# Kernel optimization log

Hardware: AMD Instinct MI355X
Metric: run time of the kernel (lower is better)

Reference implementation:

```python
import jax, jax.numpy as jnp
import numpy as np

G, N, EPG = 32, 128, 2048   # graphs, nodes/graph (uniform), edges/graph
H, L = 128, 2               # hidden_dim, num_layers
OUT = 12


def setup_inputs() -> dict:
    key = jax.random.key(0)
    ks = jax.random.split(key, 32)
    x = jax.random.randint(ks[0], (G * N, 9), 0, 2, dtype=jnp.int32)
    edge_attr = jax.random.randint(ks[1], (G * EPG, 3), 0, 2, dtype=jnp.int32)
    # edges stay within their own graph (global ids = local + graph offset)
    src = jax.random.randint(ks[2], (G, EPG), 0, N, dtype=jnp.int32)
    dst = jax.random.randint(ks[3], (G, EPG), 0, N, dtype=jnp.int32)
    off = (jnp.arange(G, dtype=jnp.int32) * N)[:, None]
    edge_index = jnp.stack([(src + off).reshape(-1), (dst + off).reshape(-1)]).astype(jnp.int64)
    batch_idx = (jnp.arange(G * N) // N).astype(jnp.int32)

    def p(k, shape, scale=0.05):
        return jax.random.normal(k, shape, dtype=jnp.float32) * scale

    return dict(
        x=x, edge_index=edge_index, edge_attr=edge_attr, batch_idx=batch_idx,
        atom_tab=p(ks[4], (9, 119, H)), bond_tab=p(ks[5], (3, 8, H)),
        W_m1=p(ks[6], (L, 2 * H, H)), b_m1=jnp.zeros((L, H), jnp.float32),
        W_m2=p(ks[7], (L, 2 * H, H)), b_m2=jnp.zeros((L, H), jnp.float32),
        W_me=p(ks[8], (L, H, H)), b_me=jnp.zeros((L, H), jnp.float32),
        W_mg=p(ks[9], (L, H, H)), b_mg=jnp.zeros((L, H), jnp.float32),
        W_h1=p(ks[10], (L, H, H)), b_h1=jnp.zeros((L, H), jnp.float32),
        W_h2=p(ks[11], (L, H, H)), b_h2=jnp.zeros((L, H), jnp.float32),
        W_o1=p(ks[12], (L, 2 * H, H)), b_o1=jnp.zeros((L, H), jnp.float32),
        W_o2=p(ks[13], (L, H, H)), b_o2=jnp.zeros((L, H), jnp.float32),
        Wg1=p(ks[14], (H, H)), bg1=jnp.zeros((H,), jnp.float32),
        Wg2=p(ks[15], (H, OUT)), bg2=jnp.zeros((OUT,), jnp.float32),
    )


def reference(x, edge_index, edge_attr, batch_idx, atom_tab, bond_tab,
              W_m1, b_m1, W_m2, b_m2, W_me, b_me, W_mg, b_mg,
              W_h1, b_h1, W_h2, b_h2, W_o1, b_o1, W_o2, b_o2,
              Wg1, bg1, Wg2, bg2):
    # Atom/Bond encoders: sum of per-feature embeddings
    node_fts = jnp.sum(jax.vmap(lambda t, i: t[i], in_axes=(0, 1))(atom_tab, x), axis=0)        # (G*N, H)
    edge_fts = jnp.sum(jax.vmap(lambda t, i: t[i], in_axes=(0, 1))(bond_tab, edge_attr), axis=0)  # (E, H)

    # dense adjacency + dense edge features (one fused scatter, replaces per-graph loop)
    g = (edge_index[0] // N).astype(jnp.int32)
    s = (edge_index[0] % N).astype(jnp.int32)
    d = (edge_index[1] % N).astype(jnp.int32)
    adj = jnp.zeros((G, N, N), jnp.float32).at[g, s, d].set(1.0)
    edense = jnp.zeros((G, N, N, H), jnp.float32).at[g, s, d].set(edge_fts)

    nd = node_fts.reshape(G, N, H)          # to_dense_batch (uniform graphs -> no padding)
    gf = jnp.zeros((G, H), jnp.float32)
    hid = jnp.zeros_like(nd)
    NEG = jnp.float32(-1e9)

    for l in range(L):  # CLRS MPNN layers
        z = jnp.concatenate([nd, hid], axis=-1)                 # (G, N, 2H)
        m1 = z @ W_m1[l] + b_m1[l]
        m2 = z @ W_m2[l] + b_m2[l]
        me = edense @ W_me[l] + b_me[l]                         # (G, N, N, H)
        mg = gf @ W_mg[l] + b_mg[l]
        msgs = m1[:, None, :, :] + m2[:, :, None, :] + me + mg[:, None, None, :]
        h = jax.nn.relu(msgs)
        h = jax.nn.relu(h @ W_h1[l] + b_h1[l]) @ W_h2[l] + b_h2[l]
        h = jnp.where(adj[..., None] > 0, h, NEG)               # masked max over senders
        agg = jnp.max(h, axis=1)                                # (G, N, H)
        hid = jax.nn.relu(z @ W_o1[l] + b_o1[l] + agg @ W_o2[l] + b_o2[l])

    emb = hid.mean(axis=1)                                      # (G, H)
    return jax.nn.relu(emb @ Wg1 + bg1) @ Wg2 + bg2             # (G, OUT)
```

## Files before the change

kernel.cpp:

```cpp
#include <hip/hip_runtime.h>

#define Gg   32
#define Nn   128
#define Hh   128
#define Ee   65536
#define GN   4096
#define GNN  524288

typedef unsigned short ushort_t;
typedef __attribute__((ext_vector_type(8))) __bf16 bf16x8;
typedef __attribute__((ext_vector_type(4))) float f32x4;
struct us4 { ushort_t a, b, c, d; };

__device__ __forceinline__ float reluf(float x) { return x > 0.f ? x : 0.f; }

__device__ __forceinline__ unsigned fkey(float f) {
  unsigned u = __float_as_uint(f);
  return (u & 0x80000000u) ? ~u : (u | 0x80000000u);
}
__device__ __forceinline__ float funkey(unsigned k) {
  unsigned u = (k & 0x80000000u) ? (k ^ 0x80000000u) : ~k;
  return __uint_as_float(u);
}

__device__ __forceinline__ ushort_t bfh(float x) {
  unsigned u = __float_as_uint(x);
  return (ushort_t)((u + 0x7FFFu + ((u >> 16) & 1u)) >> 16);
}
__device__ __forceinline__ void split2(float x, ushort_t& h, ushort_t& l) {
  h = bfh(x);
  float hf = __uint_as_float(((unsigned)h) << 16);
  l = bfh(x - hf);
}

__global__ __launch_bounds__(128) void k_detect(const int* __restrict__ e32,
                                                int* __restrict__ flag) {
  __shared__ int s;
  if (threadIdx.x == 0) s = 0;
  __syncthreads();
  if (e32[2 * threadIdx.x + 1] != 0) atomicOr(&s, 1);
  __syncthreads();
  if (threadIdx.x == 0) *flag = s;
}

__global__ __launch_bounds__(256) void k_node_encode(const int* __restrict__ x,
                                                     const float* __restrict__ atom_tab,
                                                     float* __restrict__ nf,
                                                     float* __restrict__ hid) {
  int t = blockIdx.x * 256 + threadIdx.x;
  int v = t >> 7, h = t & 127;
  float s = 0.f;
#pragma unroll
  for (int f = 0; f < 9; ++f) {
    int idx = x[v * 9 + f];
    s += atom_tab[(f * 119 + idx) * Hh + h];
  }
  nf[t] = s;
  hid[t] = 0.f;
}

__global__ __launch_bounds__(256) void k_bond_fts(const float* __restrict__ bond_tab,
                                                  float* __restrict__ bf) {
  int t = blockIdx.x * 256 + threadIdx.x;
  int c = t >> 7, h = t & 127;
  int a0 = c & 7, a1 = (c >> 3) & 7, a2 = (c >> 6) & 7;
  bf[t] = bond_tab[(0 * 8 + a0) * Hh + h] + bond_tab[(1 * 8 + a1) * Hh + h] +
          bond_tab[(2 * 8 + a2) * Hh + h];
}

__global__ __launch_bounds__(256) void k_scatter_win(const int* __restrict__ e32,
                                                     const int* __restrict__ flag,
                                                     int* __restrict__ win) {
  int e = blockIdx.x * 256 + threadIdx.x;
  int sg, dg;
  if (*flag) { sg = e32[e]; dg = e32[Ee + e]; }
  else       { sg = e32[2 * e]; dg = e32[2 * Ee + 2 * e]; }
  int g = sg / Nn;
  int s = sg % Nn;
  int d = dg % Nn;
  atomicMax(&win[(g * Nn + d) * Nn + s], e);
}

__global__ __launch_bounds__(256) void k_dcount(const int* __restrict__ win,
                                                int* __restrict__ dcnt) {
  int tid = threadIdx.x;
  int grp = tid >> 7, t = tid & 127;
  int dest = blockIdx.x * 2 + grp;
  bool valid = win[dest * 128 + t] >= 0;
  unsigned long long mask = __ballot(valid);
  __shared__ int cw[4];
  if ((tid & 63) == 0) cw[tid >> 6] = __popcll(mask);
  __syncthreads();
  if (t == 0) dcnt[dest] = cw[grp * 2] + cw[grp * 2 + 1];
}

__global__ __launch_bounds__(512) void k_dscan(const int* __restrict__ dcnt,
                                               int* __restrict__ rowptr) {
  int tid = threadIdx.x;
  int c0, c1, c2, c3, c4, c5, c6, c7;
  int bi = tid * 8;
  c0 = dcnt[bi + 0]; c1 = dcnt[bi + 1]; c2 = dcnt[bi + 2]; c3 = dcnt[bi + 3];
  c4 = dcnt[bi + 4]; c5 = dcnt[bi + 5]; c6 = dcnt[bi + 6]; c7 = dcnt[bi + 7];
  int s = c0 + c1 + c2 + c3 + c4 + c5 + c6 + c7;
  int x = s;
#pragma unroll
  for (int off = 1; off < 64; off <<= 1) {
    int y = __shfl_up(x, off, 64);
    if ((tid & 63) >= off) x += y;
  }
  __shared__ int wsum[8], woff[8];
  if ((tid & 63) == 63) wsum[tid >> 6] = x;
  __syncthreads();
  if (tid == 0) {
    int a = 0;
#pragma unroll
    for (int i = 0; i < 8; ++i) { woff[i] = a; a += wsum[i]; }
  }
  __syncthreads();
  int base = x - s + woff[tid >> 6];
  rowptr[bi + 0] = base; base += c0;
  rowptr[bi + 1] = base; base += c1;
  rowptr[bi + 2] = base; base += c2;
  rowptr[bi + 3] = base; base += c3;
  rowptr[bi + 4] = base; base += c4;
  rowptr[bi + 5] = base; base += c5;
  rowptr[bi + 6] = base; base += c6;
  rowptr[bi + 7] = base; base += c7;
  if (tid == 511) rowptr[4096] = base;
}

__global__ __launch_bounds__(256) void k_dfill(const int* __restrict__ win,
                                               const int* __restrict__ eattr,
                                               const int* __restrict__ rowptr,
                                               unsigned* __restrict__ recs) {
  int tid = threadIdx.x;
  int grp = tid >> 7, t = tid & 127;
  int dest = blockIdx.x * 2 + grp;
  int e = win[dest * 128 + t];
  bool valid = e >= 0;
  unsigned long long mask = __ballot(valid);
  __shared__ int cw[4];
  int lane = tid & 63;
  if (lane == 0) cw[tid >> 6] = __popcll(mask);
  __syncthreads();
  if (valid) {
    int off = __popcll(mask & ((1ull << lane) - 1));
    if ((tid >> 6) & 1) off += cw[grp * 2];
    int a0 = eattr[e * 3 + 0], a1 = eattr[e * 3 + 1], a2 = eattr[e * 3 + 2];
    unsigned code = (unsigned)(a0 + (a1 << 3) + (a2 << 6));
    unsigned idx = ((unsigned)dest << 7) | (unsigned)t;
    recs[rowptr[dest] + off] = (idx << 9) | code;
  }
}


__global__ __launch_bounds__(256) void k_wprep(const float* __restrict__ W_h1,
                                               const float* __restrict__ W_h2,
                                               ushort_t* __restrict__ wt) {
  int t = blockIdx.x * 256 + threadIdx.x;
  int l = t >> 15;
  int m = (t >> 14) & 1;
  int e = t & 16383;
  int n = e & 127, k = e >> 7;
  const float* W = (m == 0 ? W_h1 : W_h2) + l * 16384;
  float v = W[k * 128 + n];
  ushort_t h, lo;
  split2(v, h, lo);
  int nf = n >> 4, lr = n & 15, kf = k >> 5, lg = (k >> 3) & 3, j = k & 7;
  int off = ((nf * 4 + kf) * 64 + lg * 16 + lr) * 8 + j;
  int base = ((l * 2 + m) * 2) * 16384;
  wt[base + off] = h;
  wt[base + 16384 + off] = lo;
}

__global__ __launch_bounds__(256) void k_wprep_o(const float* __restrict__ W_o1,
                                                 const float* __restrict__ W_o2,
                                                 ushort_t* __restrict__ wo) {
  int e = blockIdx.x * 256 + threadIdx.x;
  int l = blockIdx.y;
  int n = e / 384, k = e - n * 384;
  float v = (k < 256) ? W_o1[(l * 256 + k) * 128 + n]
                      : W_o2[(l * 128 + (k - 256)) * 128 + n];
  ushort_t h, lo;
  split2(v, h, lo);
  int nf = n >> 4, lr = n & 15, kf = k >> 5, lg = (k >> 3) & 3, j = k & 7;
  int off = ((nf * 12 + kf) * 64 + lg * 16 + lr) * 8 + j;
  wo[(l * 2 + 0) * 49152 + off] = h;
  wo[(l * 2 + 1) * 49152 + off] = lo;
}

__global__ __launch_bounds__(256) void k_wprep_m(const float* __restrict__ W_m1,
                                                 const float* __restrict__ W_m2,
                                                 ushort_t* __restrict__ wm) {
  int t = blockIdx.x * 256 + threadIdx.x;
  int l = t >> 16;
  int m = (t >> 15) & 1;
  int e = t & 32767;
  int n = e >> 8, k = e & 255;
  const float* W = (m == 0 ? W_m1 : W_m2);
  float v = W[(l * 256 + k) * 128 + n];
  ushort_t h, lo;
  split2(v, h, lo);
  int nf = n >> 4, lr = n & 15, kf = k >> 5, lg = (k >> 3) & 3, j = k & 7;
  int off = ((nf * 8 + kf) * 64 + lg * 16 + lr) * 8 + j;
  int base = ((l * 2 + m) * 2) * 32768;
  wm[base + off] = h;
  wm[base + 32768 + off] = lo;
}

__global__ __launch_bounds__(256) void k_me_init(const float* __restrict__ bf,
                                                 const float* __restrict__ W_me,
                                                 const float* __restrict__ b_me,
                                                 const float* __restrict__ b_mg,
                                                 float* __restrict__ me,
                                                 unsigned* __restrict__ aggk) {
  __shared__ float v[2][128];
  int tid = threadIdx.x;
  int half = tid >> 7, j = tid & 127;
  int c = blockIdx.x * 2 + half;
  v[half][j] = bf[c * 128 + j];
  __syncthreads();
  float acc = b_me[j] + b_mg[j];
  for (int i = 0; i < 128; ++i) acc += v[half][i] * W_me[i * 128 + j];
  me[c * 128 + j] = acc;
  unsigned key = fkey(-1.0e9f);
#pragma unroll
  for (int i = 0; i < 8; ++i) aggk[blockIdx.x * 2048 + i * 256 + tid] = key;
}

__global__ __launch_bounds__(256) void k_m12(const float* __restrict__ nf_,
                                             const float* __restrict__ hid,
                                             const ushort_t* __restrict__ wm,
                                             const float* __restrict__ bi1,
                                             const float* __restrict__ bi2,
                                             float* __restrict__ m1,
                                             float* __restrict__ m2) {
  __shared__ ushort_t AH[16][264];
  __shared__ ushort_t AL[16][264];
  int tid = threadIdx.x;
  int v0 = blockIdx.x * 16;
#pragma unroll
  for (int i = 0; i < 4; ++i) {
    int idx = tid + i * 256;
    int row = idx >> 6, c4 = idx & 63;
    float4 v = (c4 < 32) ? ((const float4*)nf_)[(v0 + row) * 32 + c4]
                         : ((const float4*)hid)[(v0 + row) * 32 + (c4 - 32)];
    us4 h4, l4;
    split2(v.x, h4.a, l4.a); split2(v.y, h4.b, l4.b);
    split2(v.z, h4.c, l4.c); split2(v.w, h4.d, l4.d);
    *(us4*)&AH[row][c4 * 4] = h4;
    *(us4*)&AL[row][c4 * 4] = l4;
  }
  __syncthreads();
  int lane = tid & 63, wid = tid >> 6;
  int lr = lane & 15, lg = lane >> 4;
  f32x4 a1[2], a2[2];
#pragma unroll
  for (int i = 0; i < 2; ++i) { a1[i] = (f32x4){0.f,0.f,0.f,0.f}; a2[i] = (f32x4){0.f,0.f,0.f,0.f}; }
  const ushort_t* w1h = wm;
  const ushort_t* w1l = wm + 32768;
  const ushort_t* w2h = wm + 65536;
  const ushort_t* w2l = wm + 98304;
#pragma unroll
  for (int seg = 0; seg < 2; ++seg) {
    bf16x8 ah[4], al[4];
#pragma unroll
    for (int kf = 0; kf < 4; ++kf) {
      ah[kf] = *(const bf16x8*)&AH[lr][seg * 128 + lg * 8 + 32 * kf];
      al[kf] = *(const bf16x8*)&AL[lr][seg * 128 + lg * 8 + 32 * kf];
    }
#pragma unroll
    for (int jj = 0; jj < 2; ++jj) {
      int nfr = 2 * wid + jj;
#pragma unroll
      for (int kf = 0; kf < 4; ++kf) {
        int ch = ((nfr * 8 + seg * 4 + kf) << 9) + lane * 8;
        bf16x8 b1h = *(const bf16x8*)(w1h + ch);
        bf16x8 b1l = *(const bf16x8*)(w1l + ch);
        bf16x8 b2h = *(const bf16x8*)(w2h + ch);
        bf16x8 b2l = *(const bf16x8*)(w2l + ch);
        a1[jj] = __builtin_amdgcn_mfma_f32_16x16x32_bf16(ah[kf], b1h, a1[jj], 0, 0, 0);
        a1[jj] = __builtin_amdgcn_mfma_f32_16x16x32_bf16(ah[kf], b1l, a1[jj], 0, 0, 0);
        a1[jj] = __builtin_amdgcn_mfma_f32_16x16x32_bf16(al[kf], b1h, a1[jj], 0, 0, 0);
        a2[jj] = __builtin_amdgcn_mfma_f32_16x16x32_bf16(ah[kf], b2h, a2[jj], 0, 0, 0);
        a2[jj] = __builtin_amdgcn_mfma_f32_16x16x32_bf16(ah[kf], b2l, a2[jj], 0, 0, 0);
        a2[jj] = __builtin_amdgcn_mfma_f32_16x16x32_bf16(al[kf], b2h, a2[jj], 0, 0, 0);
      }
    }
  }
#pragma unroll
  for (int jj = 0; jj < 2; ++jj) {
    int col = 16 * (2 * wid + jj) + lr;
    float bb1 = bi1[col], bb2 = bi2[col];
#pragma unroll
    for (int reg = 0; reg < 4; ++reg) {
      int row = v0 + lg * 4 + reg;
      m1[row * Hh + col] = a1[jj][reg] + bb1;
      m2[row * Hh + col] = a2[jj][reg] + bb2;
    }
  }
}

__device__ __forceinline__ void load_afrag(const ushort_t (*MH)[136],
                                           const ushort_t (*ML)[136],
                                           int row, int lg,
                                           bf16x8 ah[4], bf16x8 al[4]) {
#pragma unroll
  for (int kf = 0; kf < 4; ++kf) {
    ah[kf] = *(const bf16x8*)&MH[row][lg * 8 + 32 * kf];
    al[kf] = *(const bf16x8*)&ML[row][lg * 8 + 32 * kf];
  }
}

__global__ __launch_bounds__(512) void k_edge(const unsigned* __restrict__ recs,
                                              const int* __restrict__ cnt,
                                              const float* __restrict__ m1,
                                              const float* __restrict__ m2,
                                              const float* __restrict__ me,
                                              const ushort_t* __restrict__ wt1h,
                                              const ushort_t* __restrict__ wt1l,
                                              const ushort_t* __restrict__ wt2h,
                                              const ushort_t* __restrict__ wt2l,
                                              const float* __restrict__ b_h1,
                                              const float* __restrict__ b_h2,
                                              unsigned* __restrict__ aggk) {
  __shared__ ushort_t MH[64][136];
  __shared__ ushort_t ML[64][136];
  __shared__ unsigned srec[64];
  int tid = threadIdx.x;
  int n = *cnt;
  if (tid < 64) {
    int r = blockIdx.x * 64 + tid;
    srec[tid] = (r < n) ? recs[r] : 0xFFFFFFFFu;
  }
  __syncthreads();
  {
    int c4 = tid & 31, rq = tid >> 5;
#pragma unroll
    for (int i = 0; i < 4; ++i) {
      int r = 16 * i + rq;
      float4 v = make_float4(0.f, 0.f, 0.f, 0.f);
      unsigned rec = srec[r];
      if (rec != 0xFFFFFFFFu) {
        int code = rec & 511;
        unsigned idx = rec >> 9;
        int s = idx & 127, d = (idx >> 7) & 127, g = idx >> 14;
        float4 a = *(const float4*)(m1 + (((g << 7) + d) << 7) + c4 * 4);
        float4 b = *(const float4*)(m2 + (((g << 7) + s) << 7) + c4 * 4);
        float4 cme = *(const float4*)(me + (code << 7) + c4 * 4);
        v.x = reluf(a.x + b.x + cme.x);
        v.y = reluf(a.y + b.y + cme.y);
        v.z = reluf(a.z + b.z + cme.z);
        v.w = reluf(a.w + b.w + cme.w);
      }
      us4 h4, l4;
      split2(v.x, h4.a, l4.a); split2(v.y, h4.b, l4.b);
      split2(v.z, h4.c, l4.c); split2(v.w, h4.d, l4.d);
      *(us4*)&MH[r][c4 * 4] = h4;
      *(us4*)&ML[r][c4 * 4] = l4;
    }
  }
  __syncthreads();

  int lane = tid & 63, wid = tid >> 6;
  int lr = lane & 15, lg = lane >> 4;
  float b1v = b_h1[16 * wid + lr];
  float b2v = b_h2[16 * wid + lr];
  f32x4 acc[4];
#pragma unroll
  for (int rg = 0; rg < 4; ++rg) acc[rg] = (f32x4){0.f, 0.f, 0.f, 0.f};
#pragma unroll
  for (int rg = 0; rg < 4; ++rg) {
    bf16x8 ah[4], al[4];
    load_afrag(MH, ML, 16 * rg + lr, lg, ah, al);
#pragma unroll
    for (int kf = 0; kf < 4; ++kf) {
      int ch = ((wid * 4 + kf) << 9) + lane * 8;
      bf16x8 bh = *(const bf16x8*)(wt1h + ch);
      bf16x8 bl = *(const bf16x8*)(wt1l + ch);
      acc[rg] = __builtin_amdgcn_mfma_f32_16x16x32_bf16(ah[kf], bh, acc[rg], 0, 0, 0);
      acc[rg] = __builtin_amdgcn_mfma_f32_16x16x32_bf16(ah[kf], bl, acc[rg], 0, 0, 0);
      acc[rg] = __builtin_amdgcn_mfma_f32_16x16x32_bf16(al[kf], bh, acc[rg], 0, 0, 0);
    }
  }
  __syncthreads();
#pragma unroll
  for (int rg = 0; rg < 4; ++rg)
#pragma unroll
    for (int reg = 0; reg < 4; ++reg) {
      float t = reluf(acc[rg][reg] + b1v);
      int row = 16 * rg + lg * 4 + reg;
      int col = 16 * wid + lr;
      ushort_t h, l;
      split2(t, h, l);
      MH[row][col] = h;
      ML[row][col] = l;
    }
  __syncthreads();
#pragma unroll
  for (int rg = 0; rg < 4; ++rg) acc[rg] = (f32x4){0.f, 0.f, 0.f, 0.f};
#pragma unroll
  for (int rg = 0; rg < 4; ++rg) {
    bf16x8 ah[4], al[4];
    load_afrag(MH, ML, 16 * rg + lr, lg, ah, al);
#pragma unroll
    for (int kf = 0; kf < 4; ++kf) {
      int ch = ((wid * 4 + kf) << 9) + lane * 8;
      bf16x8 bh = *(const bf16x8*)(wt2h + ch);
      bf16x8 bl = *(const bf16x8*)(wt2l + ch);
      acc[rg] = __builtin_amdgcn_mfma_f32_16x16x32_bf16(ah[kf], bh, acc[rg], 0, 0, 0);
      acc[rg] = __builtin_amdgcn_mfma_f32_16x16x32_bf16(ah[kf], bl, acc[rg], 0, 0, 0);
      acc[rg] = __builtin_amdgcn_mfma_f32_16x16x32_bf16(al[kf], bh, acc[rg], 0, 0, 0);
    }
  }
  __syncthreads();
#pragma unroll
  for (int rg = 0; rg < 4; ++rg)
#pragma unroll
    for (int reg = 0; reg < 4; ++reg) {
      int row = 16 * rg + lg * 4 + reg;
      int col = 16 * wid + lr;
      unsigned b = __float_as_uint(acc[rg][reg] + b2v);
      MH[row][col] = (ushort_t)(b >> 16);
      ML[row][col] = (ushort_t)(b & 0xFFFFu);
    }
  __syncthreads();
  {
    int c = tid & 127, quarter = tid >> 7;
    int rbeg = quarter * 16, rend = rbeg + 16;
    unsigned curkey = 0xFFFFu;
    float best = -3.0e38f;
    for (int r = rbeg; r < rend; ++r) {
      unsigned rec = srec[r];
      unsigned key = rec >> 16;
      if (key != curkey) {
        if (curkey != 0xFFFFu)
          atomicMax(aggk + (curkey << 7) + c, fkey(best));
        curkey = key;
        best = -3.0e38f;
      }
      if (key != 0xFFFFu) {
        unsigned b = ((unsigned)MH[r][c] << 16) | (unsigned)ML[r][c];
        best = fmaxf(best, __uint_as_float(b));
      }
    }
    if (curkey != 0xFFFFu)
      atomicMax(aggk + (curkey << 7) + c, fkey(best));
  }
}

__global__ __launch_bounds__(256) void k_out(const float* __restrict__ nf,
                                             const float* __restrict__ hid,
                                             const unsigned* __restrict__ aggk,
                                             const ushort_t* __restrict__ wo_h,
                                             const ushort_t* __restrict__ wo_l,
                                             const float* __restrict__ bo1,
                                             const float* __restrict__ bo2,
                                             float* __restrict__ hidn) {
  __shared__ ushort_t MH[16][136];
  __shared__ ushort_t ML[16][136];
  int tid = threadIdx.x;
  int v0 = blockIdx.x * 16;
  int lane = tid & 63, wid = tid >> 6;
  int lr = lane & 15, lg = lane >> 4;
  f32x4 acc[2];
#pragma unroll
  for (int jj = 0; jj < 2; ++jj) acc[jj] = (f32x4){0.f, 0.f, 0.f, 0.f};

  for (int seg = 0; seg < 3; ++seg) {
#pragma unroll
    for (int i = 0; i < 2; ++i) {
      int idx = tid + i * 256;
      int row = idx >> 5, c4 = idx & 31;
      float4 v;
      if (seg == 0)      v = ((const float4*)nf)[(v0 + row) * 32 + c4];
      else if (seg == 1) v = ((const float4*)hid)[(v0 + row) * 32 + c4];
      else {
        uint4 k4 = ((const uint4*)aggk)[(v0 + row) * 32 + c4];
        v.x = funkey(k4.x); v.y = funkey(k4.y); v.z = funkey(k4.z); v.w = funkey(k4.w);
      }
      us4 h4, l4;
      split2(v.x, h4.a, l4.a);
      split2(v.y, h4.b, l4.b);
      split2(v.z, h4.c, l4.c);
      split2(v.w, h4.d, l4.d);
      *(us4*)&MH[row][c4 * 4] = h4;
      *(us4*)&ML[row][c4 * 4] = l4;
    }
    __syncthreads();
    bf16x8 ah[4], al[4];
    load_afrag(MH, ML, lr, lg, ah, al);
#pragma unroll
    for (int jj = 0; jj < 2; ++jj) {
      int nfr = 2 * wid + jj;
#pragma unroll
      for (int kf = 0; kf < 4; ++kf) {
        int ch = ((nfr * 12 + seg * 4 + kf) << 9) + lane * 8;
        bf16x8 bh = *(const bf16x8*)(wo_h + ch);
        bf16x8 bl = *(const bf16x8*)(wo_l + ch);
        acc[jj] = __builtin_amdgcn_mfma_f32_16x16x32_bf16(ah[kf], bh, acc[jj], 0, 0, 0);
        acc[jj] = __builtin_amdgcn_mfma_f32_16x16x32_bf16(ah[kf], bl, acc[jj], 0, 0, 0);
        acc[jj] = __builtin_amdgcn_mfma_f32_16x16x32_bf16(al[kf], bh, acc[jj], 0, 0, 0);
      }
    }
    __syncthreads();
  }
#pragma unroll
  for (int jj = 0; jj < 2; ++jj) {
    int col = 16 * (2 * wid + jj) + lr;
    float b = bo1[col] + bo2[col];
#pragma unroll
    for (int reg = 0; reg < 4; ++reg)
      hidn[(v0 + lg * 4 + reg) * Hh + col] = reluf(acc[jj][reg] + b);
  }
}

__global__ __launch_bounds__(128) void k_head(const float* __restrict__ hid,
                                              const float* __restrict__ Wg1,
                                              const float* __restrict__ bg1,
                                              const float* __restrict__ Wg2,
                                              const float* __restrict__ bg2,
                                              float* __restrict__ out) {
  __shared__ float emb[Hh];
  __shared__ float tt[Hh];
  int g = blockIdx.x, j = threadIdx.x;
  float s = 0.f;
  for (int n = 0; n < Nn; ++n) s += hid[(g * Nn + n) * Hh + j];
  emb[j] = s * (1.f / Nn);
  __syncthreads();
  float a = bg1[j];
  for (int i = 0; i < Hh; ++i) a += emb[i] * Wg1[i * Hh + j];
  tt[j] = reluf(a);
  __syncthreads();
  if (j < 12) {
    float o = bg2[j];
    for (int i = 0; i < Hh; ++i) o += tt[i] * Wg2[i * 12 + j];
    out[g * 12 + j] = o;
  }
}

extern "C" void kernel_launch(void* const* d_in, const int* in_sizes, int n_in,
                              void* d_out, int out_size, void* d_ws, size_t ws_size,
                              hipStream_t stream) {
  const int* x = (const int*)d_in[0];
  const int* eidx32 = (const int*)d_in[1];
  const int* eattr = (const int*)d_in[2];
  const float* atom_tab = (const float*)d_in[4];
  const float* bond_tab = (const float*)d_in[5];
  const float* W_m1 = (const float*)d_in[6];
  const float* b_m1 = (const float*)d_in[7];
  const float* W_m2 = (const float*)d_in[8];
  const float* b_m2 = (const float*)d_in[9];
  const float* W_me = (const float*)d_in[10];
  const float* b_me = (const float*)d_in[11];
  const float* b_mg = (const float*)d_in[13];
  const float* W_h1 = (const float*)d_in[14];
  const float* b_h1 = (const float*)d_in[15];
  const float* W_h2 = (const float*)d_in[16];
  const float* b_h2 = (const float*)d_in[17];
  const float* W_o1 = (const float*)d_in[18];
  const float* b_o1 = (const float*)d_in[19];
  const float* W_o2 = (const float*)d_in[20];
  const float* b_o2 = (const float*)d_in[21];
  const float* Wg1 = (const float*)d_in[22];
  const float* bg1 = (const float*)d_in[23];
  const float* Wg2 = (const float*)d_in[24];
  const float* bg2 = (const float*)d_in[25];
  float* out = (float*)d_out;

  char* ws = (char*)d_ws;
  float* nf = (float*)(ws);
  float* hidA = (float*)(ws + (2u << 20));
  float* hidB = (float*)(ws + (4u << 20));
  float* m1 = (float*)(ws + (6u << 20));
  float* m2 = (float*)(ws + (8u << 20));
  unsigned* aggk = (unsigned*)(ws + (10u << 20));
  int* win = (int*)(ws + (12u << 20));
  ushort_t* wo = (ushort_t*)(ws + (12u << 20));
  ushort_t* wm = (ushort_t*)(ws + (12u << 20) + 393216);
  ushort_t* wt = (ushort_t*)(ws + (14u << 20));
  float* bf = (float*)(ws + (14u << 20) + (256u << 10));
  float* me = (float*)(ws + (14u << 20) + (512u << 10));
  unsigned* recs = (unsigned*)(ws + (14u << 20) + (768u << 10));
  int* dcnt = (int*)(ws + (15u << 20));
  int* rowptr = (int*)(ws + (15u << 20) + (16u << 10));
  int* eflag = (int*)(ws + (15u << 20) + (48u << 10));

  hipMemsetAsync(win, 0xFF, GNN * sizeof(int), stream);
  k_detect<<<1, 128, 0, stream>>>(eidx32, eflag);
  k_node_encode<<<2048, 256, 0, stream>>>(x, atom_tab, nf, hidA);
  k_bond_fts<<<256, 256, 0, stream>>>(bond_tab, bf);
  k_scatter_win<<<256, 256, 0, stream>>>(eidx32, eflag, win);
  k_dcount<<<2048, 256, 0, stream>>>(win, dcnt);
  k_dscan<<<1, 512, 0, stream>>>(dcnt, rowptr);
  k_dfill<<<2048, 256, 0, stream>>>(win, eattr, rowptr, recs);
  k_wprep<<<256, 256, 0, stream>>>(W_h1, W_h2, wt);
  k_wprep_o<<<dim3(192, 2), 256, 0, stream>>>(W_o1, W_o2, wo);
  k_wprep_m<<<512, 256, 0, stream>>>(W_m1, W_m2, wm);

  int* cnt = rowptr + 4096;

  float* hc = hidA;
  float* hn = hidB;
  for (int l = 0; l < 2; ++l) {
    const ushort_t* wt1h = wt + ((l * 2 + 0) * 2 + 0) * 16384;
    const ushort_t* wt1l = wt + ((l * 2 + 0) * 2 + 1) * 16384;
    const ushort_t* wt2h = wt + ((l * 2 + 1) * 2 + 0) * 16384;
    const ushort_t* wt2l = wt + ((l * 2 + 1) * 2 + 1) * 16384;
    const ushort_t* wo_h = wo + (l * 2 + 0) * 49152;
    const ushort_t* wo_l = wo + (l * 2 + 1) * 49152;
    k_me_init<<<256, 256, 0, stream>>>(bf, W_me + l * Hh * Hh, b_me + l * Hh,
                                       b_mg + l * Hh, me, aggk);
    k_m12<<<256, 256, 0, stream>>>(nf, hc, wm + l * 131072, b_m1 + l * Hh,
                                   b_m2 + l * Hh, m1, m2);
    k_edge<<<1024, 512, 0, stream>>>(recs, cnt, m1, m2, me, wt1h, wt1l, wt2h, wt2l,
                                     b_h1 + l * Hh, b_h2 + l * Hh, aggk);
    k_out<<<256, 256, 0, stream>>>(nf, hc, aggk, wo_h, wo_l,
                                   b_o1 + l * Hh, b_o2 + l * Hh, hn);
    float* t = hc; hc = hn; hn = t;
  }
  k_head<<<32, 128, 0, stream>>>(hc, Wg1, bg1, Wg2, bg2, out);
}
```

Before: 134.2 us.

## Fuse node encode with m12, batch per-layer me init, fuse k_out with next-layer m12

Merges the node encoder into the layer-0 m1/m2 GEMM. That kernel exploits hid=0 and only multiplies the nf half of the weights. Both layers' edge-embedding projections and agg-key initialisations move into one launch with separate buffers. Layer 0's output projection is fused with layer 1's m1/m2 GEMM so the new hidden state is reused from shared memory. Together this cuts kernel launches and global round-trips, at the cost of more workspace and a hand-unrolled layer loop.

```diff
diff --git a/kernel.cpp b/kernel.cpp
--- a/kernel.cpp
+++ b/kernel.cpp
@@ -41,22 +41,6 @@
   if (e32[2 * threadIdx.x + 1] != 0) atomicOr(&s, 1);
   __syncthreads();
   if (threadIdx.x == 0) *flag = s;
-}
-
-__global__ __launch_bounds__(256) void k_node_encode(const int* __restrict__ x,
-                                                     const float* __restrict__ atom_tab,
-                                                     float* __restrict__ nf,
-                                                     float* __restrict__ hid) {
-  int t = blockIdx.x * 256 + threadIdx.x;
-  int v = t >> 7, h = t & 127;
-  float s = 0.f;
-#pragma unroll
-  for (int f = 0; f < 9; ++f) {
-    int idx = x[v * 9 + f];
-    s += atom_tab[(f * 119 + idx) * Hh + h];
-  }
-  nf[t] = s;
-  hid[t] = 0.f;
 }
 
 __global__ __launch_bounds__(256) void k_bond_fts(const float* __restrict__ bond_tab,
@@ -208,48 +192,89 @@
   wm[base + 32768 + off] = lo;
 }
 
-__global__ __launch_bounds__(256) void k_me_init(const float* __restrict__ bf,
-                                                 const float* __restrict__ W_me,
-                                                 const float* __restrict__ b_me,
-                                                 const float* __restrict__ b_mg,
-                                                 float* __restrict__ me,
-                                                 unsigned* __restrict__ aggk) {
+__global__ __launch_bounds__(256) void k_me2(const float* __restrict__ bf,
+                                             const float* __restrict__ W_me,
+                                             const float* __restrict__ b_me,
+                                             const float* __restrict__ b_mg,
+                                             float* __restrict__ me0,
+                                             float* __restrict__ me1,
+                                             unsigned* __restrict__ aggkA,
+                                             unsigned* __restrict__ aggkB) {
+  int bx = blockIdx.x;
+  int l = bx >> 8, b2 = bx & 255;
+  const float* W = W_me + l * 16384;
+  const float* bme = b_me + l * 128;
+  const float* bmg = b_mg + l * 128;
+  float* me = l ? me1 : me0;
+  unsigned* aggk = l ? aggkB : aggkA;
   __shared__ float v[2][128];
   int tid = threadIdx.x;
   int half = tid >> 7, j = tid & 127;
-  int c = blockIdx.x * 2 + half;
+  int c = b2 * 2 + half;
   v[half][j] = bf[c * 128 + j];
   __syncthreads();
-  float acc = b_me[j] + b_mg[j];
-  for (int i = 0; i < 128; ++i) acc += v[half][i] * W_me[i * 128 + j];
+  float acc = bme[j] + bmg[j];
+  for (int i = 0; i < 128; ++i) acc += v[half][i] * W[i * 128 + j];
   me[c * 128 + j] = acc;
   unsigned key = fkey(-1.0e9f);
 #pragma unroll
-  for (int i = 0; i < 8; ++i) aggk[blockIdx.x * 2048 + i * 256 + tid] = key;
-}
-
-__global__ __launch_bounds__(256) void k_m12(const float* __restrict__ nf_,
-                                             const float* __restrict__ hid,
-                                             const ushort_t* __restrict__ wm,
-                                             const float* __restrict__ bi1,
-                                             const float* __restrict__ bi2,
-                                             float* __restrict__ m1,
-                                             float* __restrict__ m2) {
-  __shared__ ushort_t AH[16][264];
-  __shared__ ushort_t AL[16][264];
+  for (int i = 0; i < 8; ++i) aggk[b2 * 2048 + i * 256 + tid] = key;
+}
+
+__device__ __forceinline__ void load_afrag(const ushort_t (*MH)[136],
+                                           const ushort_t (*ML)[136],
+                                           int row, int lg,
+                                           bf16x8 ah[4], bf16x8 al[4]) {
+#pragma unroll
+  for (int kf = 0; kf < 4; ++kf) {
+    ah[kf] = *(const bf16x8*)&MH[row][lg * 8 + 32 * kf];
+    al[kf] = *(const bf16x8*)&ML[row][lg * 8 + 32 * kf];
+  }
+}
+
+__device__ __forceinline__ void load_afrag264(const ushort_t (*MH)[264],
+                                              const ushort_t (*ML)[264],
+                                              int row, int base, int lg,
+                                              bf16x8 ah[4], bf16x8 al[4]) {
+#pragma unroll
+  for (int kf = 0; kf < 4; ++kf) {
+    ah[kf] = *(const bf16x8*)&MH[row][base + lg * 8 + 32 * kf];
+    al[kf] = *(const bf16x8*)&ML[row][base + lg * 8 + 32 * kf];
+  }
+}
+
+__global__ __launch_bounds__(256) void k_encode_m12(const int* __restrict__ x,
+                                                    const float* __restrict__ atom_tab,
+                                                    const ushort_t* __restrict__ wm,
+                                                    const float* __restrict__ bi1,
+                                                    const float* __restrict__ bi2,
+                                                    float* __restrict__ nf_,
+                                                    float* __restrict__ hid,
+                                                    float* __restrict__ m1,
+                                                    float* __restrict__ m2) {
+  __shared__ ushort_t AH[16][136];
+  __shared__ ushort_t AL[16][136];
+  __shared__ int xs[144];
   int tid = threadIdx.x;
   int v0 = blockIdx.x * 16;
-#pragma unroll
-  for (int i = 0; i < 4; ++i) {
-    int idx = tid + i * 256;
-    int row = idx >> 6, c4 = idx & 63;
-    float4 v = (c4 < 32) ? ((const float4*)nf_)[(v0 + row) * 32 + c4]
-                         : ((const float4*)hid)[(v0 + row) * 32 + (c4 - 32)];
-    us4 h4, l4;
-    split2(v.x, h4.a, l4.a); split2(v.y, h4.b, l4.b);
-    split2(v.z, h4.c, l4.c); split2(v.w, h4.d, l4.d);
-    *(us4*)&AH[row][c4 * 4] = h4;
-    *(us4*)&AL[row][c4 * 4] = l4;
+  if (tid < 144) xs[tid] = x[v0 * 9 + tid];
+  __syncthreads();
+#pragma unroll
+  for (int i = 0; i < 8; ++i) {
+    int e = tid + i * 256;
+    int row = e >> 7, col = e & 127;
+    float s = 0.f;
+#pragma unroll
+    for (int f = 0; f < 9; ++f) {
+      int idx = xs[row * 9 + f];
+      s += atom_tab[(f * 119 + idx) * Hh + col];
+    }
+    nf_[(v0 + row) * Hh + col] = s;
+    hid[(v0 + row) * Hh + col] = 0.f;
+    ushort_t h, l;
+    split2(s, h, l);
+    AH[row][col] = h;
+    AL[row][col] = l;
   }
   __syncthreads();
   int lane = tid & 63, wid = tid >> 6;
@@ -261,31 +286,24 @@
   const ushort_t* w1l = wm + 32768;
   const ushort_t* w2h = wm + 65536;
   const ushort_t* w2l = wm + 98304;
-#pragma unroll
-  for (int seg = 0; seg < 2; ++seg) {
-    bf16x8 ah[4], al[4];
+  bf16x8 ah[4], al[4];
+  load_afrag(AH, AL, lr, lg, ah, al);
+#pragma unroll
+  for (int jj = 0; jj < 2; ++jj) {
+    int nfr = 2 * wid + jj;
 #pragma unroll
     for (int kf = 0; kf < 4; ++kf) {
-      ah[kf] = *(const bf16x8*)&AH[lr][seg * 128 + lg * 8 + 32 * kf];
-      al[kf] = *(const bf16x8*)&AL[lr][seg * 128 + lg * 8 + 32 * kf];
-    }
-#pragma unroll
-    for (int jj = 0; jj < 2; ++jj) {
-      int nfr = 2 * wid + jj;
-#pragma unroll
-      for (int kf = 0; kf < 4; ++kf) {
-        int ch = ((nfr * 8 + seg * 4 + kf) << 9) + lane * 8;
-        bf16x8 b1h = *(const bf16x8*)(w1h + ch);
-        bf16x8 b1l = *(const bf16x8*)(w1l + ch);
-        bf16x8 b2h = *(const bf16x8*)(w2h + ch);
-        bf16x8 b2l = *(const bf16x8*)(w2l + ch);
-        a1[jj] = __builtin_amdgcn_mfma_f32_16x16x32_bf16(ah[kf], b1h, a1[jj], 0, 0, 0);
-        a1[jj] = __builtin_amdgcn_mfma_f32_16x16x32_bf16(ah[kf], b1l, a1[jj], 0, 0, 0);
-        a1[jj] = __builtin_amdgcn_mfma_f32_16x16x32_bf16(al[kf], b1h, a1[jj], 0, 0, 0);
-        a2[jj] = __builtin_amdgcn_mfma_f32_16x16x32_bf16(ah[kf], b2h, a2[jj], 0, 0, 0);
-        a2[jj] = __builtin_amdgcn_mfma_f32_16x16x32_bf16(ah[kf], b2l, a2[jj], 0, 0, 0);
-        a2[jj] = __builtin_amdgcn_mfma_f32_16x16x32_bf16(al[kf], b2h, a2[jj], 0, 0, 0);
-      }
+      int ch = ((nfr * 8 + kf) << 9) + lane * 8;
+      bf16x8 b1h = *(const bf16x8*)(w1h + ch);
+      bf16x8 b1l = *(const bf16x8*)(w1l + ch);
+      bf16x8 b2h = *(const bf16x8*)(w2h + ch);
+      bf16x8 b2l = *(const bf16x8*)(w2l + ch);
+      a1[jj] = __builtin_amdgcn_mfma_f32_16x16x32_bf16(ah[kf], b1h, a1[jj], 0, 0, 0);
+      a1[jj] = __builtin_amdgcn_mfma_f32_16x16x32_bf16(ah[kf], b1l, a1[jj], 0, 0, 0);
+      a1[jj] = __builtin_amdgcn_mfma_f32_16x16x32_bf16(al[kf], b1h, a1[jj], 0, 0, 0);
+      a2[jj] = __builtin_amdgcn_mfma_f32_16x16x32_bf16(ah[kf], b2h, a2[jj], 0, 0, 0);
+      a2[jj] = __builtin_amdgcn_mfma_f32_16x16x32_bf16(ah[kf], b2l, a2[jj], 0, 0, 0);
+      a2[jj] = __builtin_amdgcn_mfma_f32_16x16x32_bf16(al[kf], b2h, a2[jj], 0, 0, 0);
     }
   }
 #pragma unroll
@@ -298,17 +316,6 @@
       m1[row * Hh + col] = a1[jj][reg] + bb1;
       m2[row * Hh + col] = a2[jj][reg] + bb2;
     }
-  }
-}
-
-__device__ __forceinline__ void load_afrag(const ushort_t (*MH)[136],
-                                           const ushort_t (*ML)[136],
-                                           int row, int lg,
-                                           bf16x8 ah[4], bf16x8 al[4]) {
-#pragma unroll
-  for (int kf = 0; kf < 4; ++kf) {
-    ah[kf] = *(const bf16x8*)&MH[row][lg * 8 + 32 * kf];
-    al[kf] = *(const bf16x8*)&ML[row][lg * 8 + 32 * kf];
   }
 }
 
@@ -512,6 +519,139 @@
 #pragma unroll
     for (int reg = 0; reg < 4; ++reg)
       hidn[(v0 + lg * 4 + reg) * Hh + col] = reluf(acc[jj][reg] + b);
+  }
+}
+
+__global__ __launch_bounds__(256) void k_out_m12(const float* __restrict__ nf,
+                                                 const float* __restrict__ hid,
+                                                 const unsigned* __restrict__ aggk,
+                                                 const ushort_t* __restrict__ wo_h,
+                                                 const ushort_t* __restrict__ wo_l,
+                                                 const float* __restrict__ bo1,
+                                                 const float* __restrict__ bo2,
+                                                 const ushort_t* __restrict__ wm,
+                                                 const float* __restrict__ bm1,
+                                                 const float* __restrict__ bm2,
+                                                 float* __restrict__ hidn,
+                                                 float* __restrict__ m1,
+                                                 float* __restrict__ m2) {
+  __shared__ ushort_t AH[16][264];
+  __shared__ ushort_t AL[16][264];
+  int tid = threadIdx.x;
+  int v0 = blockIdx.x * 16;
+  int lane = tid & 63, wid = tid >> 6;
+  int lr = lane & 15, lg = lane >> 4;
+  f32x4 acc[2];
+#pragma unroll
+  for (int jj = 0; jj < 2; ++jj) acc[jj] = (f32x4){0.f, 0.f, 0.f, 0.f};
+
+  for (int seg = 0; seg < 3; ++seg) {
+#pragma unroll
+    for (int i = 0; i < 2; ++i) {
+      int idx = tid + i * 256;
+      int row = idx >> 5, c4 = idx & 31;
+      float4 v;
+      if (seg == 0)      v = ((const float4*)nf)[(v0 + row) * 32 + c4];
+      else if (seg == 1) v = ((const float4*)hid)[(v0 + row) * 32 + c4];
+      else {
+        uint4 k4 = ((const uint4*)aggk)[(v0 + row) * 32 + c4];
+        v.x = funkey(k4.x); v.y = funkey(k4.y); v.z = funkey(k4.z); v.w = funkey(k4.w);
+      }
+      us4 h4, l4;
+      split2(v.x, h4.a, l4.a);
+      split2(v.y, h4.b, l4.b);
+      split2(v.z, h4.c, l4.c);
+      split2(v.w, h4.d, l4.d);
+      *(us4*)&AH[row][c4 * 4] = h4;
+      *(us4*)&AL[row][c4 * 4] = l4;
+    }
+    __syncthreads();
+    bf16x8 ah[4], al[4];
+    load_afrag264(AH, AL, lr, 0, lg, ah, al);
+#pragma unroll
+    for (int jj = 0; jj < 2; ++jj) {
+      int nfr = 2 * wid + jj;
+#pragma unroll
+      for (int kf = 0; kf < 4; ++kf) {
+        int ch = ((nfr * 12 + seg * 4 + kf) << 9) + lane * 8;
+        bf16x8 bh = *(const bf16x8*)(wo_h + ch);
+        bf16x8 bl = *(const bf16x8*)(wo_l + ch);
+        acc[jj] = __builtin_amdgcn_mfma_f32_16x16x32_bf16(ah[kf], bh, acc[jj], 0, 0, 0);
+        acc[jj] = __builtin_amdgcn_mfma_f32_16x16x32_bf16(ah[kf], bl, acc[jj], 0, 0, 0);
+        acc[jj] = __builtin_amdgcn_mfma_f32_16x16x32_bf16(al[kf], bh, acc[jj], 0, 0, 0);
+      }
+    }
+    __syncthreads();
+  }
+#pragma unroll
+  for (int jj = 0; jj < 2; ++jj) {
+    int col = 16 * (2 * wid + jj) + lr;
+    float b = bo1[col] + bo2[col];
+#pragma unroll
+    for (int reg = 0; reg < 4; ++reg) {
+      float hv = reluf(acc[jj][reg] + b);
+      int row = lg * 4 + reg;
+      hidn[(v0 + row) * Hh + col] = hv;
+      ushort_t h, l;
+      split2(hv, h, l);
+      AH[row][128 + col] = h;
+      AL[row][128 + col] = l;
+    }
+  }
+#pragma unroll
+  for (int i = 0; i < 2; ++i) {
+    int idx = tid + i * 256;
+    int row = idx >> 5, c4 = idx & 31;
+    float4 v = ((const float4*)nf)[(v0 + row) * 32 + c4];
+    us4 h4, l4;
+    split2(v.x, h4.a, l4.a);
+    split2(v.y, h4.b, l4.b);
+    split2(v.z, h4.c, l4.c);
+    split2(v.w, h4.d, l4.d);
+    *(us4*)&AH[row][c4 * 4] = h4;
+    *(us4*)&AL[row][c4 * 4] = l4;
+  }
+  __syncthreads();
+  f32x4 a1[2], a2[2];
+#pragma unroll
+  for (int i = 0; i < 2; ++i) { a1[i] = (f32x4){0.f,0.f,0.f,0.f}; a2[i] = (f32x4){0.f,0.f,0.f,0.f}; }
+  const ushort_t* w1h = wm;
+  const ushort_t* w1l = wm + 32768;
+  const ushort_t* w2h = wm + 65536;
+  const ushort_t* w2l = wm + 98304;
+#pragma unroll
+  for (int seg = 0; seg < 2; ++seg) {
+    bf16x8 ah[4], al[4];
+    load_afrag264(AH, AL, lr, seg * 128, lg, ah, al);
+#pragma unroll
+    for (int jj = 0; jj < 2; ++jj) {
+      int nfr = 2 * wid + jj;
+#pragma unroll
+      for (int kf = 0; kf < 4; ++kf) {
+        int ch = ((nfr * 8 + seg * 4 + kf) << 9) + lane * 8;
+        bf16x8 b1h = *(const bf16x8*)(w1h + ch);
+        bf16x8 b1l = *(const bf16x8*)(w1l + ch);
+        bf16x8 b2h = *(const bf16x8*)(w2h + ch);
+        bf16x8 b2l = *(const bf16x8*)(w2l + ch);
+        a1[jj] = __builtin_amdgcn_mfma_f32_16x16x32_bf16(ah[kf], b1h, a1[jj], 0, 0, 0);
+        a1[jj] = __builtin_amdgcn_mfma_f32_16x16x32_bf16(ah[kf], b1l, a1[jj], 0, 0, 0);
+        a1[jj] = __builtin_amdgcn_mfma_f32_16x16x32_bf16(al[kf], b1h, a1[jj], 0, 0, 0);
+        a2[jj] = __builtin_amdgcn_mfma_f32_16x16x32_bf16(ah[kf], b2h, a2[jj], 0, 0, 0);
+        a2[jj] = __builtin_amdgcn_mfma_f32_16x16x32_bf16(ah[kf], b2l, a2[jj], 0, 0, 0);
+        a2[jj] = __builtin_amdgcn_mfma_f32_16x16x32_bf16(al[kf], b2h, a2[jj], 0, 0, 0);
+      }
+    }
+  }
+#pragma unroll
+  for (int jj = 0; jj < 2; ++jj) {
+    int col = 16 * (2 * wid + jj) + lr;
+    float bb1 = bm1[col], bb2 = bm2[col];
+#pragma unroll
+    for (int reg = 0; reg < 4; ++reg) {
+      int row = v0 + lg * 4 + reg;
+      m1[row * Hh + col] = a1[jj][reg] + bb1;
+      m2[row * Hh + col] = a2[jj][reg] + bb2;
+    }
   }
 }
 
@@ -574,50 +714,51 @@
   float* hidB = (float*)(ws + (4u << 20));
   float* m1 = (float*)(ws + (6u << 20));
   float* m2 = (float*)(ws + (8u << 20));
-  unsigned* aggk = (unsigned*)(ws + (10u << 20));
+  unsigned* aggkA = (unsigned*)(ws + (10u << 20));
   int* win = (int*)(ws + (12u << 20));
-  ushort_t* wo = (ushort_t*)(ws + (12u << 20));
-  ushort_t* wm = (ushort_t*)(ws + (12u << 20) + 393216);
   ushort_t* wt = (ushort_t*)(ws + (14u << 20));
   float* bf = (float*)(ws + (14u << 20) + (256u << 10));
-  float* me = (float*)(ws + (14u << 20) + (512u << 10));
-  unsigned* recs = (unsigned*)(ws + (14u << 20) + (768u << 10));
-  int* dcnt = (int*)(ws + (15u << 20));
-  int* rowptr = (int*)(ws + (15u << 20) + (16u << 10));
-  int* eflag = (int*)(ws + (15u << 20) + (48u << 10));
+  float* me0 = (float*)(ws + (14u << 20) + (512u << 10));
+  float* me1 = (float*)(ws + (14u << 20) + (768u << 10));
+  unsigned* recs = (unsigned*)(ws + (15u << 20));
+  int* dcnt = (int*)(ws + (15u << 20) + (256u << 10));
+  int* rowptr = (int*)(ws + (15u << 20) + (272u << 10));
+  int* eflag = (int*)(ws + (15u << 20) + (304u << 10));
+  unsigned* aggkB = (unsigned*)(ws + (16u << 20));
+  ushort_t* wo = (ushort_t*)(ws + (18u << 20));
+  ushort_t* wm = (ushort_t*)(ws + (18u << 20) + (512u << 10));
 
   hipMemsetAsync(win, 0xFF, GNN * sizeof(int), stream);
   k_detect<<<1, 128, 0, stream>>>(eidx32, eflag);
-  k_node_encode<<<2048, 256, 0, stream>>>(x, atom_tab, nf, hidA);
   k_bond_fts<<<256, 256, 0, stream>>>(bond_tab, bf);
+  k_wprep<<<256, 256, 0, stream>>>(W_h1, W_h2, wt);
+  k_wprep_o<<<dim3(192, 2), 256, 0, stream>>>(W_o1, W_o2, wo);
+  k_wprep_m<<<512, 256, 0, stream>>>(W_m1, W_m2, wm);
+  k_me2<<<512, 256, 0, stream>>>(bf, W_me, b_me, b_mg, me0, me1, aggkA, aggkB);
+  k_encode_m12<<<256, 256, 0, stream>>>(x, atom_tab, wm, b_m1, b_m2,
+                                        nf, hidA, m1, m2);
   k_scatter_win<<<256, 256, 0, stream>>>(eidx32, eflag, win);
   k_dcount<<<2048, 256, 0, stream>>>(win, dcnt);
   k_dscan<<<1, 512, 0, stream>>>(dcnt, rowptr);
   k_dfill<<<2048, 256, 0, stream>>>(win, eattr, rowptr, recs);
-  k_wprep<<<256, 256, 0, stream>>>(W_h1, W_h2, wt);
-  k_wprep_o<<<dim3(192, 2), 256, 0, stream>>>(W_o1, W_o2, wo);
-  k_wprep_m<<<512, 256, 0, stream>>>(W_m1, W_m2, wm);
 
   int* cnt = rowptr + 4096;
 
-  float* hc = hidA;
-  float* hn = hidB;
-  for (int l = 0; l < 2; ++l) {
-    const ushort_t* wt1h = wt + ((l * 2 + 0) * 2 + 0) * 16384;
-    const ushort_t* wt1l = wt + ((l * 2 + 0) * 2 + 1) * 16384;
-    const ushort_t* wt2h = wt + ((l * 2 + 1) * 2 + 0) * 16384;
-    const ushort_t* wt2l = wt + ((l * 2 + 1) * 2 + 1) * 16384;
-    const ushort_t* wo_h = wo + (l * 2 + 0) * 49152;
-    const ushort_t* wo_l = wo + (l * 2 + 1) * 49152;
-    k_me_init<<<256, 256, 0, stream>>>(bf, W_me + l * Hh * Hh, b_me + l * Hh,
-                                       b_mg + l * Hh, me, aggk);
-    k_m12<<<256, 256, 0, stream>>>(nf, hc, wm + l * 131072, b_m1 + l * Hh,
-                                   b_m2 + l * Hh, m1, m2);
-    k_edge<<<1024, 512, 0, stream>>>(recs, cnt, m1, m2, me, wt1h, wt1l, wt2h, wt2l,
-                                     b_h1 + l * Hh, b_h2 + l * Hh, aggk);
-    k_out<<<256, 256, 0, stream>>>(nf, hc, aggk, wo_h, wo_l,
-                                   b_o1 + l * Hh, b_o2 + l * Hh, hn);
-    float* t = hc; hc = hn; hn = t;
-  }
-  k_head<<<32, 128, 0, stream>>>(hc, Wg1, bg1, Wg2, bg2, out);
-}
+  k_edge<<<1024, 512, 0, stream>>>(recs, cnt, m1, m2, me0,
+                                   wt + 0 * 16384, wt + 1 * 16384,
+                                   wt + 2 * 16384, wt + 3 * 16384,
+                                   b_h1, b_h2, aggkA);
+  k_out_m12<<<256, 256, 0, stream>>>(nf, hidA, aggkA,
+                                     wo + 0 * 49152, wo + 1 * 49152,
+                                     b_o1, b_o2,
+                                     wm + 131072, b_m1 + Hh, b_m2 + Hh,
+                                     hidB, m1, m2);
+  k_edge<<<1024, 512, 0, stream>>>(recs, cnt, m1, m2, me1,
+                                   wt + 4 * 16384, wt + 5 * 16384,
+                                   wt + 6 * 16384, wt + 7 * 16384,
+                                   b_h1 + Hh, b_h2 + Hh, aggkB);
+  k_out<<<256, 256, 0, stream>>>(nf, hidB, aggkB,
+                                 wo + 2 * 49152, wo + 3 * 49152,
+                                 b_o1 + Hh, b_o2 + Hh, hidA);
+  k_head<<<32, 128, 0, stream>>>(hidA, Wg1, bg1, Wg2, bg2, out);
+}
```

After: 127.6 us. 4.9% less time.
